# Kernel tuning notes

Hardware: AMD Instinct MI355X
Metric: run time of the kernel (lower is better)

## Reference

```python
import jax, jax.numpy as jnp
import numpy as np

B, T, D = 2, 4096, 2048
H, DI = 4, 64

def setup_inputs() -> dict:
    key = jax.random.key(0)
    k1, k2, k3, k4 = jax.random.split(key, 4)
    x = jax.random.normal(k1, (B, T, D), dtype=jnp.float32)
    # nn.Linear(in, out) weight applied as x @ W with W shaped [in, out]
    Wq = jax.random.normal(k2, (D, H * DI), dtype=jnp.float32) * (1.0 / np.sqrt(D))
    Wk = jax.random.normal(k3, (D, DI), dtype=jnp.float32) * (1.0 / np.sqrt(D))
    Ww = jax.random.normal(k4, (D, H), dtype=jnp.float32) * (1.0 / np.sqrt(D))
    return {"x": x, "Wq": Wq, "Wk": Wk, "Ww": Ww}

def reference(x, Wq, Wk, Ww):
    Bv, Tv, _ = x.shape
    queries = (x @ Wq).reshape(Bv, Tv, H, DI)   # [B,T,H,DI]
    keys = x @ Wk                                # [B,S,DI]
    weights = x @ Ww                             # [B,T,H]
    dots = jnp.einsum('bthd,bsd->bths', queries, keys)  # [B,T,H,S]
    activated = jax.nn.relu(dots)
    # per-head weight then head-reduction: sum_h w[b,t,h] * relu(dots)[b,t,h,s]
    index_scores = jnp.einsum('bths,bth->bts', activated, weights)
    return index_scores
```

## Files before the change

### kernel.cpp

```cpp
#include <hip/hip_runtime.h>
#include <hip/hip_bf16.h>

#define Bdim 2
#define Tdim 4096
#define Ddim 2048
#define Hdim 4
#define DIdim 64
#define NQ 256
#define NCAT 324
#define NPAD 384
#define Mdim 8192

typedef __attribute__((ext_vector_type(8))) short bf16x8;
typedef __attribute__((ext_vector_type(4))) float f32x4;

__device__ __forceinline__ unsigned short f2bf(float f) {
    unsigned int u = __builtin_bit_cast(unsigned int, f);
    u += 0x7fffu + ((u >> 16) & 1u);
    return (unsigned short)(u >> 16);
}
__device__ __forceinline__ float bf2f(unsigned short h) {
    unsigned int u = ((unsigned int)h) << 16;
    return __builtin_bit_cast(float, u);
}

__global__ __launch_bounds__(256) void pack_w(const float* __restrict__ Wq,
                                              const float* __restrict__ Wk,
                                              const float* __restrict__ Ww,
                                              unsigned short* __restrict__ WcatT) {
    const int n0 = blockIdx.x * 64;
    const int d0 = blockIdx.y * 64;
    __shared__ float tile[64][65];
    const int t = threadIdx.x;
#pragma unroll
    for (int i = 0; i < 16; ++i) {
        int flat = i * 256 + t;
        int r = flat >> 6;
        int c = flat & 63;
        int n = n0 + c, d = d0 + r;
        float v;
        if (n < NQ)            v = Wq[(size_t)d * NQ + n];
        else if (n < NQ + 64)  v = Wk[(size_t)d * DIdim + (n - NQ)];
        else if (n < NCAT)     v = Ww[(size_t)d * Hdim + (n - NQ - 64)];
        else                   v = 0.0f;
        tile[r][c] = v;
    }
    __syncthreads();
#pragma unroll
    for (int i = 0; i < 16; ++i) {
        int flat = i * 256 + t;
        int nn = flat >> 6;
        int dd = flat & 63;
        WcatT[(size_t)(n0 + nn) * Ddim + d0 + dd] = f2bf(tile[dd][nn]);
    }
}

#define BM 128
#define BN 64
#define BK 64

__global__ __launch_bounds__(256) void proj_gemm(const float* __restrict__ x,
                                                 const unsigned short* __restrict__ WcatT,
                                                 unsigned short* __restrict__ QKW) {
    __shared__ __align__(16) unsigned char lds[BM * BK * 2 + BN * BK * 2];
    const int m0 = blockIdx.y * BM;
    const int n0 = blockIdx.x * BN;
    const int tid = threadIdx.x;
    const int lane = tid & 63;
    const int wave = tid >> 6;

    f32x4 acc[2][4];
#pragma unroll
    for (int ts = 0; ts < 2; ++ts)
#pragma unroll
        for (int ns = 0; ns < 4; ++ns)
            acc[ts][ns] = (f32x4){0.f, 0.f, 0.f, 0.f};

    const int lrow = lane & 15;
    const int kgrp = lane >> 4;

    for (int k0 = 0; k0 < Ddim; k0 += BK) {
        __syncthreads();
#pragma unroll
        for (int i = 0; i < 8; ++i) {
            int flat = i * 256 + tid;
            int r = flat >> 4;
            int c4 = flat & 15;
            const float4 v = *reinterpret_cast<const float4*>(
                &x[(size_t)(m0 + r) * Ddim + k0 + c4 * 4]);
            unsigned int p0 = (unsigned int)f2bf(v.x) | ((unsigned int)f2bf(v.y) << 16);
            unsigned int p1 = (unsigned int)f2bf(v.z) | ((unsigned int)f2bf(v.w) << 16);
            int byte = r * 128 + c4 * 8;
            byte ^= (r & 7) << 4;
            *reinterpret_cast<uint2*>(&lds[byte]) = make_uint2(p0, p1);
        }
#pragma unroll
        for (int i = 0; i < 2; ++i) {
            int flat = i * 256 + tid;
            int n = flat >> 3;
            int k8 = flat & 7;
            const int4 v = *reinterpret_cast<const int4*>(
                &WcatT[(size_t)(n0 + n) * Ddim + k0 + k8 * 8]);
            int byte = n * 128 + k8 * 16;
            byte ^= (n & 7) << 4;
            *reinterpret_cast<int4*>(&lds[BM * BK * 2 + byte]) = v;
        }
        __syncthreads();
#pragma unroll
        for (int ks = 0; ks < 2; ++ks) {
            bf16x8 a[2], bb[4];
#pragma unroll
            for (int ts = 0; ts < 2; ++ts) {
                int r = wave * 32 + ts * 16 + lrow;
                int byte = r * 128 + (ks * 32 + 8 * kgrp) * 2;
                byte ^= (r & 7) << 4;
                a[ts] = *reinterpret_cast<const bf16x8*>(&lds[byte]);
            }
#pragma unroll
            for (int ns = 0; ns < 4; ++ns) {
                int n = ns * 16 + lrow;
                int byte = n * 128 + (ks * 32 + 8 * kgrp) * 2;
                byte ^= (n & 7) << 4;
                bb[ns] = *reinterpret_cast<const bf16x8*>(&lds[BM * BK * 2 + byte]);
            }
#pragma unroll
            for (int ts = 0; ts < 2; ++ts)
#pragma unroll
                for (int ns = 0; ns < 4; ++ns)
                    acc[ts][ns] = __builtin_amdgcn_mfma_f32_16x16x32_bf16(
                        a[ts], bb[ns], acc[ts][ns], 0, 0, 0);
        }
    }
#pragma unroll
    for (int ts = 0; ts < 2; ++ts)
#pragma unroll
        for (int ns = 0; ns < 4; ++ns)
#pragma unroll
            for (int j = 0; j < 4; ++j) {
                int r = m0 + wave * 32 + ts * 16 + kgrp * 4 + j;
                int c = n0 + ns * 16 + lrow;
                QKW[(size_t)r * NPAD + c] = f2bf(acc[ts][ns][j]);
            }
}

__global__ __launch_bounds__(256) void indexer(const unsigned short* __restrict__ QKW,
                                               float* __restrict__ out) {
    const int st = blockIdx.x;
    const int tt = blockIdx.y;
    const int b  = blockIdx.z;
    const int tid = threadIdx.x;
    const int lane = tid & 63;
    const int wave = tid >> 6;
    const int lrow = lane & 15;
    const int kgrp = lane >> 4;
    const int kcol = 8 * kgrp;

    bf16x8 kf[8][2];
#pragma unroll
    for (int ss = 0; ss < 8; ++ss)
#pragma unroll
        for (int ks = 0; ks < 2; ++ks) {
            size_t row = (size_t)(b * Tdim + st * 128 + ss * 16 + lrow);
            kf[ss][ks] = *reinterpret_cast<const bf16x8*>(
                &QKW[row * NPAD + NQ + ks * 32 + kcol]);
        }

    float wreg[2][4][4];
#pragma unroll
    for (int ts = 0; ts < 2; ++ts)
#pragma unroll
        for (int j = 0; j < 4; ++j) {
            int t = tt * 128 + wave * 32 + ts * 16 + kgrp * 4 + j;
            const unsigned short* wp = &QKW[(size_t)(b * Tdim + t) * NPAD + NQ + 64];
#pragma unroll
            for (int h = 0; h < Hdim; ++h) wreg[ts][j][h] = bf2f(wp[h]);
        }

    f32x4 oacc[2][8];
#pragma unroll
    for (int ts = 0; ts < 2; ++ts)
#pragma unroll
        for (int ss = 0; ss < 8; ++ss)
            oacc[ts][ss] = (f32x4){0.f, 0.f, 0.f, 0.f};

#pragma unroll
    for (int h = 0; h < Hdim; ++h) {
        bf16x8 qf[2][2];
#pragma unroll
        for (int ts = 0; ts < 2; ++ts)
#pragma unroll
            for (int ks = 0; ks < 2; ++ks) {
                size_t row = (size_t)(b * Tdim + tt * 128 + wave * 32 + ts * 16 + lrow);
                qf[ts][ks] = *reinterpret_cast<const bf16x8*>(
                    &QKW[row * NPAD + h * DIdim + ks * 32 + kcol]);
            }
#pragma unroll
        for (int ss = 0; ss < 8; ++ss) {
            f32x4 d[2];
            d[0] = (f32x4){0.f, 0.f, 0.f, 0.f};
            d[1] = (f32x4){0.f, 0.f, 0.f, 0.f};
#pragma unroll
            for (int ks = 0; ks < 2; ++ks)
#pragma unroll
                for (int ts = 0; ts < 2; ++ts)
                    d[ts] = __builtin_amdgcn_mfma_f32_16x16x32_bf16(
                        qf[ts][ks], kf[ss][ks], d[ts], 0, 0, 0);
#pragma unroll
            for (int ts = 0; ts < 2; ++ts)
#pragma unroll
                for (int j = 0; j < 4; ++j)
                    oacc[ts][ss][j] += wreg[ts][j][h] * fmaxf(d[ts][j], 0.f);
        }
    }

#pragma unroll
    for (int ts = 0; ts < 2; ++ts)
#pragma unroll
        for (int ss = 0; ss < 8; ++ss)
#pragma unroll
            for (int j = 0; j < 4; ++j) {
                int t = tt * 128 + wave * 32 + ts * 16 + kgrp * 4 + j;
                int s = st * 128 + ss * 16 + lrow;
                out[((size_t)b * Tdim + t) * Tdim + s] = oacc[ts][ss][j];
            }
}

extern "C" void kernel_launch(void* const* d_in, const int* in_sizes, int n_in,
                              void* d_out, int out_size, void* d_ws, size_t ws_size,
                              hipStream_t stream) {
    const float* x  = (const float*)d_in[0];
    const float* Wq = (const float*)d_in[1];
    const float* Wk = (const float*)d_in[2];
    const float* Ww = (const float*)d_in[3];
    float* out = (float*)d_out;

    unsigned short* WcatT = (unsigned short*)d_ws;
    unsigned short* QKW   = (unsigned short*)((char*)d_ws + (size_t)NPAD * Ddim * 2);

    pack_w<<<dim3(NPAD / 64, Ddim / 64), 256, 0, stream>>>(Wq, Wk, Ww, WcatT);
    proj_gemm<<<dim3(NPAD / BN, Mdim / BM), 256, 0, stream>>>(x, WcatT, QKW);
    indexer<<<dim3(Tdim / 128, Tdim / 128, Bdim), 256, 0, stream>>>(QKW, out);
}
```

Measured before the change: 260.6 us.

## Pre-convert x to bf16, async LDS-load projection GEMM, split indexer across 8 waves

Adds a separate kernel that converts x to bf16 once into workspace, and a new projection GEMM that stages tiles with global_load_lds direct-to-LDS copies using a 32x192 tile. The indexer now runs 512 threads, with each wave covering half the s-range; Q fragments for all heads are hoisted into registers, weights are read as one vector load, and output uses nontemporal stores. This is meant to cut conversion work inside the GEMM inner loop and improve indexer occupancy and write behaviour. In exchange it adds an extra pass over x and needs more workspace; the old GEMM is kept as a fallback when workspace is too small.

```diff
diff --git a/kernel.cpp b/kernel.cpp
--- a/kernel.cpp
+++ b/kernel.cpp
@@ -22,6 +22,28 @@
 __device__ __forceinline__ float bf2f(unsigned short h) {
     unsigned int u = ((unsigned int)h) << 16;
     return __builtin_bit_cast(float, u);
+}
+
+__device__ __forceinline__ void gload16(const void* g, void* l) {
+    __builtin_amdgcn_global_load_lds(
+        (const __attribute__((address_space(1))) unsigned int*)g,
+        (__attribute__((address_space(3))) unsigned int*)l, 16, 0, 0);
+}
+
+__global__ __launch_bounds__(256) void convert_x(const float* __restrict__ x,
+                                                 unsigned short* __restrict__ xb) {
+    const size_t N8 = (size_t)Mdim * Ddim / 8;
+    for (size_t u = (size_t)blockIdx.x * 256 + threadIdx.x; u < N8;
+         u += (size_t)gridDim.x * 256) {
+        const float4 v0 = *reinterpret_cast<const float4*>(&x[u * 8]);
+        const float4 v1 = *reinterpret_cast<const float4*>(&x[u * 8 + 4]);
+        uint4 o;
+        o.x = (unsigned int)f2bf(v0.x) | ((unsigned int)f2bf(v0.y) << 16);
+        o.y = (unsigned int)f2bf(v0.z) | ((unsigned int)f2bf(v0.w) << 16);
+        o.z = (unsigned int)f2bf(v1.x) | ((unsigned int)f2bf(v1.y) << 16);
+        o.w = (unsigned int)f2bf(v1.z) | ((unsigned int)f2bf(v1.w) << 16);
+        *reinterpret_cast<uint4*>(&xb[u * 8]) = o;
+    }
 }
 
 __global__ __launch_bounds__(256) void pack_w(const float* __restrict__ Wq,
@@ -55,30 +77,101 @@
     }
 }
 
-#define BM 128
-#define BN 64
+#define BM2 32
+#define BN2 192
 #define BK 64
 
+__global__ __launch_bounds__(256) void proj_gemm2(const unsigned short* __restrict__ xb,
+                                                  const unsigned short* __restrict__ WcatT,
+                                                  unsigned short* __restrict__ QKW) {
+    __shared__ __align__(16) unsigned char lds[(BM2 + BN2) * BK * 2];
+    const int n0 = blockIdx.x * BN2;
+    const int m0 = blockIdx.y * BM2;
+    const int tid = threadIdx.x;
+    const int lane = tid & 63;
+    const int wave = tid >> 6;
+    const int lrow = lane & 15;
+    const int kgrp = lane >> 4;
+
+    f32x4 acc[2][3];
+#pragma unroll
+    for (int ts = 0; ts < 2; ++ts)
+#pragma unroll
+        for (int ns = 0; ns < 3; ++ns)
+            acc[ts][ns] = (f32x4){0.f, 0.f, 0.f, 0.f};
+
+    for (int k0 = 0; k0 < Ddim; k0 += BK) {
+        __syncthreads();
+        {
+            int flat = tid;
+            int r = flat >> 3, c = flat & 7;
+            int cs = c ^ (r & 7);
+            gload16(&xb[(size_t)(m0 + r) * Ddim + k0 + cs * 8], &lds[flat * 16]);
+        }
+#pragma unroll
+        for (int i = 0; i < 6; ++i) {
+            int flat = i * 256 + tid;
+            int n = flat >> 3, c = flat & 7;
+            int cs = c ^ (n & 7);
+            gload16(&WcatT[(size_t)(n0 + n) * Ddim + k0 + cs * 8],
+                    &lds[BM2 * BK * 2 + flat * 16]);
+        }
+        __syncthreads();
+#pragma unroll
+        for (int ks = 0; ks < 2; ++ks) {
+            bf16x8 a[2], bb[3];
+#pragma unroll
+            for (int ts = 0; ts < 2; ++ts) {
+                int r = ts * 16 + lrow;
+                int c = (ks * 4 + kgrp) ^ (r & 7);
+                a[ts] = *reinterpret_cast<const bf16x8*>(&lds[r * 128 + c * 16]);
+            }
+#pragma unroll
+            for (int ns = 0; ns < 3; ++ns) {
+                int n = wave * 48 + ns * 16 + lrow;
+                int c = (ks * 4 + kgrp) ^ (n & 7);
+                bb[ns] = *reinterpret_cast<const bf16x8*>(
+                    &lds[BM2 * BK * 2 + n * 128 + c * 16]);
+            }
+#pragma unroll
+            for (int ts = 0; ts < 2; ++ts)
+#pragma unroll
+                for (int ns = 0; ns < 3; ++ns)
+                    acc[ts][ns] = __builtin_amdgcn_mfma_f32_16x16x32_bf16(
+                        a[ts], bb[ns], acc[ts][ns], 0, 0, 0);
+        }
+    }
+#pragma unroll
+    for (int ts = 0; ts < 2; ++ts)
+#pragma unroll
+        for (int ns = 0; ns < 3; ++ns)
+#pragma unroll
+            for (int j = 0; j < 4; ++j) {
+                int r = m0 + ts * 16 + kgrp * 4 + j;
+                int c = n0 + wave * 48 + ns * 16 + lrow;
+                QKW[(size_t)r * NPAD + c] = f2bf(acc[ts][ns][j]);
+            }
+}
+
+#define BMf 128
+#define BNf 64
 __global__ __launch_bounds__(256) void proj_gemm(const float* __restrict__ x,
                                                  const unsigned short* __restrict__ WcatT,
                                                  unsigned short* __restrict__ QKW) {
-    __shared__ __align__(16) unsigned char lds[BM * BK * 2 + BN * BK * 2];
-    const int m0 = blockIdx.y * BM;
-    const int n0 = blockIdx.x * BN;
+    __shared__ __align__(16) unsigned char lds[BMf * BK * 2 + BNf * BK * 2];
+    const int m0 = blockIdx.y * BMf;
+    const int n0 = blockIdx.x * BNf;
     const int tid = threadIdx.x;
     const int lane = tid & 63;
     const int wave = tid >> 6;
-
     f32x4 acc[2][4];
 #pragma unroll
     for (int ts = 0; ts < 2; ++ts)
 #pragma unroll
         for (int ns = 0; ns < 4; ++ns)
             acc[ts][ns] = (f32x4){0.f, 0.f, 0.f, 0.f};
-
     const int lrow = lane & 15;
     const int kgrp = lane >> 4;
-
     for (int k0 = 0; k0 < Ddim; k0 += BK) {
         __syncthreads();
 #pragma unroll
@@ -103,7 +196,7 @@
                 &WcatT[(size_t)(n0 + n) * Ddim + k0 + k8 * 8]);
             int byte = n * 128 + k8 * 16;
             byte ^= (n & 7) << 4;
-            *reinterpret_cast<int4*>(&lds[BM * BK * 2 + byte]) = v;
+            *reinterpret_cast<int4*>(&lds[BMf * BK * 2 + byte]) = v;
         }
         __syncthreads();
 #pragma unroll
@@ -121,7 +214,7 @@
                 int n = ns * 16 + lrow;
                 int byte = n * 128 + (ks * 32 + 8 * kgrp) * 2;
                 byte ^= (n & 7) << 4;
-                bb[ns] = *reinterpret_cast<const bf16x8*>(&lds[BM * BK * 2 + byte]);
+                bb[ns] = *reinterpret_cast<const bf16x8*>(&lds[BMf * BK * 2 + byte]);
             }
 #pragma unroll
             for (int ts = 0; ts < 2; ++ts)
@@ -143,59 +236,68 @@
             }
 }
 
-__global__ __launch_bounds__(256) void indexer(const unsigned short* __restrict__ QKW,
-                                               float* __restrict__ out) {
+__global__ __launch_bounds__(512) void indexer2(const unsigned short* __restrict__ QKW,
+                                                float* __restrict__ out) {
     const int st = blockIdx.x;
     const int tt = blockIdx.y;
     const int b  = blockIdx.z;
     const int tid = threadIdx.x;
     const int lane = tid & 63;
     const int wave = tid >> 6;
+    const int wt  = wave >> 1;
+    const int wsb = wave & 1;
     const int lrow = lane & 15;
     const int kgrp = lane >> 4;
     const int kcol = 8 * kgrp;
-
-    bf16x8 kf[8][2];
-#pragma unroll
-    for (int ss = 0; ss < 8; ++ss)
+    const size_t rowBase = (size_t)b * Tdim;
+
+    bf16x8 kf[4][2];
+#pragma unroll
+    for (int ss = 0; ss < 4; ++ss)
 #pragma unroll
         for (int ks = 0; ks < 2; ++ks) {
-            size_t row = (size_t)(b * Tdim + st * 128 + ss * 16 + lrow);
+            size_t row = rowBase + st * 128 + wsb * 64 + ss * 16 + lrow;
             kf[ss][ks] = *reinterpret_cast<const bf16x8*>(
                 &QKW[row * NPAD + NQ + ks * 32 + kcol]);
         }
 
+    bf16x8 qf[4][2][2];
+#pragma unroll
+    for (int h = 0; h < Hdim; ++h)
+#pragma unroll
+        for (int ts = 0; ts < 2; ++ts)
+#pragma unroll
+            for (int ks = 0; ks < 2; ++ks) {
+                size_t row = rowBase + tt * 128 + wt * 32 + ts * 16 + lrow;
+                qf[h][ts][ks] = *reinterpret_cast<const bf16x8*>(
+                    &QKW[row * NPAD + h * DIdim + ks * 32 + kcol]);
+            }
+
     float wreg[2][4][4];
 #pragma unroll
     for (int ts = 0; ts < 2; ++ts)
 #pragma unroll
         for (int j = 0; j < 4; ++j) {
-            int t = tt * 128 + wave * 32 + ts * 16 + kgrp * 4 + j;
-            const unsigned short* wp = &QKW[(size_t)(b * Tdim + t) * NPAD + NQ + 64];
-#pragma unroll
-            for (int h = 0; h < Hdim; ++h) wreg[ts][j][h] = bf2f(wp[h]);
-        }
-
-    f32x4 oacc[2][8];
-#pragma unroll
-    for (int ts = 0; ts < 2; ++ts)
-#pragma unroll
-        for (int ss = 0; ss < 8; ++ss)
+            int t = tt * 128 + wt * 32 + ts * 16 + kgrp * 4 + j;
+            const uint2 wp = *reinterpret_cast<const uint2*>(
+                &QKW[(rowBase + t) * NPAD + NQ + 64]);
+            wreg[ts][j][0] = bf2f((unsigned short)(wp.x & 0xffff));
+            wreg[ts][j][1] = bf2f((unsigned short)(wp.x >> 16));
+            wreg[ts][j][2] = bf2f((unsigned short)(wp.y & 0xffff));
+            wreg[ts][j][3] = bf2f((unsigned short)(wp.y >> 16));
+        }
+
+    f32x4 oacc[2][4];
+#pragma unroll
+    for (int ts = 0; ts < 2; ++ts)
+#pragma unroll
+        for (int ss = 0; ss < 4; ++ss)
             oacc[ts][ss] = (f32x4){0.f, 0.f, 0.f, 0.f};
 
 #pragma unroll
-    for (int h = 0; h < Hdim; ++h) {
-        bf16x8 qf[2][2];
-#pragma unroll
-        for (int ts = 0; ts < 2; ++ts)
-#pragma unroll
-            for (int ks = 0; ks < 2; ++ks) {
-                size_t row = (size_t)(b * Tdim + tt * 128 + wave * 32 + ts * 16 + lrow);
-                qf[ts][ks] = *reinterpret_cast<const bf16x8*>(
-                    &QKW[row * NPAD + h * DIdim + ks * 32 + kcol]);
-            }
-#pragma unroll
-        for (int ss = 0; ss < 8; ++ss) {
+    for (int ss = 0; ss < 4; ++ss)
+#pragma unroll
+        for (int h = 0; h < Hdim; ++h) {
             f32x4 d[2];
             d[0] = (f32x4){0.f, 0.f, 0.f, 0.f};
             d[1] = (f32x4){0.f, 0.f, 0.f, 0.f};
@@ -204,24 +306,25 @@
 #pragma unroll
                 for (int ts = 0; ts < 2; ++ts)
                     d[ts] = __builtin_amdgcn_mfma_f32_16x16x32_bf16(
-                        qf[ts][ks], kf[ss][ks], d[ts], 0, 0, 0);
+                        qf[h][ts][ks], kf[ss][ks], d[ts], 0, 0, 0);
 #pragma unroll
             for (int ts = 0; ts < 2; ++ts)
 #pragma unroll
                 for (int j = 0; j < 4; ++j)
-                    oacc[ts][ss][j] += wreg[ts][j][h] * fmaxf(d[ts][j], 0.f);
-        }
-    }
-
-#pragma unroll
-    for (int ts = 0; ts < 2; ++ts)
-#pragma unroll
-        for (int ss = 0; ss < 8; ++ss)
+                    oacc[ts][ss][j] = fmaf(wreg[ts][j][h], fmaxf(d[ts][j], 0.f),
+                                           oacc[ts][ss][j]);
+        }
+
+#pragma unroll
+    for (int ts = 0; ts < 2; ++ts)
+#pragma unroll
+        for (int ss = 0; ss < 4; ++ss)
 #pragma unroll
             for (int j = 0; j < 4; ++j) {
-                int t = tt * 128 + wave * 32 + ts * 16 + kgrp * 4 + j;
-                int s = st * 128 + ss * 16 + lrow;
-                out[((size_t)b * Tdim + t) * Tdim + s] = oacc[ts][ss][j];
+                int t = tt * 128 + wt * 32 + ts * 16 + kgrp * 4 + j;
+                int s = st * 128 + wsb * 64 + ss * 16 + lrow;
+                __builtin_nontemporal_store(oacc[ts][ss][j],
+                                            &out[(rowBase + t) * Tdim + s]);
             }
 }
 
@@ -236,8 +339,16 @@
 
     unsigned short* WcatT = (unsigned short*)d_ws;
     unsigned short* QKW   = (unsigned short*)((char*)d_ws + (size_t)NPAD * Ddim * 2);
+    const size_t qkw_bytes = (size_t)Mdim * NPAD * 2;
+    unsigned short* xb = (unsigned short*)((char*)QKW + qkw_bytes);
+    const size_t need = (size_t)NPAD * Ddim * 2 + qkw_bytes + (size_t)Mdim * Ddim * 2;
 
     pack_w<<<dim3(NPAD / 64, Ddim / 64), 256, 0, stream>>>(Wq, Wk, Ww, WcatT);
-    proj_gemm<<<dim3(NPAD / BN, Mdim / BM), 256, 0, stream>>>(x, WcatT, QKW);
-    indexer<<<dim3(Tdim / 128, Tdim / 128, Bdim), 256, 0, stream>>>(QKW, out);
-}
+    if (ws_size >= need) {
+        convert_x<<<2048, 256, 0, stream>>>(x, xb);
+        proj_gemm2<<<dim3(NPAD / BN2, Mdim / BM2), 256, 0, stream>>>(xb, WcatT, QKW);
+    } else {
+        proj_gemm<<<dim3(NPAD / BNf, Mdim / BMf), 256, 0, stream>>>(x, WcatT, QKW);
+    }
+    indexer2<<<dim3(Tdim / 128, Tdim / 128, Bdim), 512, 0, stream>>>(QKW, out);
+}
```

New measurement: 263.8 us. Within noise of the previous version (+1.2%).

## Pre-convert x to bf16, double-buffer projection GEMM with direct LDS loads, retile indexer

Applied to the files above, without the earlier changes.

Adds a separate kernel that converts x to bf16 once. The projection GEMM is rewritten with 32x192 tiles, 512 threads, and a double-buffered LDS pipeline fed by global_load_lds. The indexer now stages key tiles through LDS and splits each block across 8 waves. It also packs the head weights, raises MFMA priority and writes output with nontemporal stores. The cost is an extra launch and a full bf16 round trip of x through global memory.

```diff
diff --git a/kernel.cpp b/kernel.cpp
--- a/kernel.cpp
+++ b/kernel.cpp
@@ -22,6 +22,33 @@
 __device__ __forceinline__ float bf2f(unsigned short h) {
     unsigned int u = ((unsigned int)h) << 16;
     return __builtin_bit_cast(float, u);
+}
+__device__ __forceinline__ float wget(uint2 w, int h) {
+    unsigned int u = (h & 2) ? w.y : w.x;
+    unsigned int v = (h & 1) ? (u & 0xffff0000u) : (u << 16);
+    return __builtin_bit_cast(float, v);
+}
+
+__device__ __forceinline__ void gload16(const void* g, void* l) {
+    __builtin_amdgcn_global_load_lds(
+        (const __attribute__((address_space(1))) unsigned int*)g,
+        (__attribute__((address_space(3))) unsigned int*)l, 16, 0, 0);
+}
+
+__global__ __launch_bounds__(256) void convert_x(const float* __restrict__ x,
+                                                 unsigned short* __restrict__ xb) {
+    const size_t N8 = (size_t)Mdim * Ddim / 8;
+    for (size_t u = (size_t)blockIdx.x * 256 + threadIdx.x; u < N8;
+         u += (size_t)gridDim.x * 256) {
+        const float4 v0 = *reinterpret_cast<const float4*>(&x[u * 8]);
+        const float4 v1 = *reinterpret_cast<const float4*>(&x[u * 8 + 4]);
+        uint4 o;
+        o.x = (unsigned int)f2bf(v0.x) | ((unsigned int)f2bf(v0.y) << 16);
+        o.y = (unsigned int)f2bf(v0.z) | ((unsigned int)f2bf(v0.w) << 16);
+        o.z = (unsigned int)f2bf(v1.x) | ((unsigned int)f2bf(v1.y) << 16);
+        o.w = (unsigned int)f2bf(v1.z) | ((unsigned int)f2bf(v1.w) << 16);
+        *reinterpret_cast<uint4*>(&xb[u * 8]) = o;
+    }
 }
 
 __global__ __launch_bounds__(256) void pack_w(const float* __restrict__ Wq,
@@ -55,173 +82,173 @@
     }
 }
 
-#define BM 128
-#define BN 64
-#define BK 64
-
-__global__ __launch_bounds__(256) void proj_gemm(const float* __restrict__ x,
-                                                 const unsigned short* __restrict__ WcatT,
-                                                 unsigned short* __restrict__ QKW) {
-    __shared__ __align__(16) unsigned char lds[BM * BK * 2 + BN * BK * 2];
-    const int m0 = blockIdx.y * BM;
-    const int n0 = blockIdx.x * BN;
+#define PBM 32
+#define PBN 192
+#define PBK 64
+#define ABYTES (PBM * PBK * 2)
+#define BBYTES (PBN * PBK * 2)
+#define BUFBYTES (ABYTES + BBYTES)
+
+__global__ __launch_bounds__(512) void proj_gemm3(const unsigned short* __restrict__ xb,
+                                                  const unsigned short* __restrict__ WcatT,
+                                                  unsigned short* __restrict__ QKW) {
+    __shared__ __align__(16) unsigned char lds[2 * BUFBYTES];
+    const int n0 = blockIdx.x * PBN;
+    const int m0 = blockIdx.y * PBM;
     const int tid = threadIdx.x;
     const int lane = tid & 63;
-    const int wave = tid >> 6;
-
-    f32x4 acc[2][4];
-#pragma unroll
-    for (int ts = 0; ts < 2; ++ts)
-#pragma unroll
-        for (int ns = 0; ns < 4; ++ns)
-            acc[ts][ns] = (f32x4){0.f, 0.f, 0.f, 0.f};
-
+    const int wm = (tid >> 6) >> 2;
+    const int wn = (tid >> 6) & 3;
     const int lrow = lane & 15;
     const int kgrp = lane >> 4;
 
-    for (int k0 = 0; k0 < Ddim; k0 += BK) {
+    f32x4 acc[3];
+#pragma unroll
+    for (int ns = 0; ns < 3; ++ns) acc[ns] = (f32x4){0.f, 0.f, 0.f, 0.f};
+
+    auto stage = [&](unsigned char* buf, int k0) {
+        if (tid < 256) {
+            int r = tid >> 3, c = tid & 7;
+            int cs = c ^ (r & 7);
+            gload16(&xb[(size_t)(m0 + r) * Ddim + k0 + cs * 8], buf + tid * 16);
+        }
+#pragma unroll
+        for (int i = 0; i < 3; ++i) {
+            int flat = i * 512 + tid;
+            int n = flat >> 3, c = flat & 7;
+            int cs = c ^ (n & 7);
+            gload16(&WcatT[(size_t)(n0 + n) * Ddim + k0 + cs * 8],
+                    buf + ABYTES + flat * 16);
+        }
+    };
+
+    stage(lds, 0);
+    __syncthreads();
+    int cur = 0;
+    for (int k0 = 0; k0 < Ddim; k0 += PBK) {
+        unsigned char* bc = lds + cur * BUFBYTES;
+        unsigned char* bn = lds + (cur ^ 1) * BUFBYTES;
+        if (k0 + PBK < Ddim) stage(bn, k0 + PBK);
+#pragma unroll
+        for (int ks = 0; ks < 2; ++ks) {
+            int r = wm * 16 + lrow;
+            int ca = (ks * 4 + kgrp) ^ (r & 7);
+            bf16x8 a = *reinterpret_cast<const bf16x8*>(bc + r * 128 + ca * 16);
+            bf16x8 bb[3];
+#pragma unroll
+            for (int ns = 0; ns < 3; ++ns) {
+                int n = wn * 48 + ns * 16 + lrow;
+                int cb = (ks * 4 + kgrp) ^ (n & 7);
+                bb[ns] = *reinterpret_cast<const bf16x8*>(bc + ABYTES + n * 128 + cb * 16);
+            }
+#pragma unroll
+            for (int ns = 0; ns < 3; ++ns)
+                acc[ns] = __builtin_amdgcn_mfma_f32_16x16x32_bf16(a, bb[ns], acc[ns], 0, 0, 0);
+        }
         __syncthreads();
-#pragma unroll
-        for (int i = 0; i < 8; ++i) {
-            int flat = i * 256 + tid;
-            int r = flat >> 4;
-            int c4 = flat & 15;
-            const float4 v = *reinterpret_cast<const float4*>(
-                &x[(size_t)(m0 + r) * Ddim + k0 + c4 * 4]);
-            unsigned int p0 = (unsigned int)f2bf(v.x) | ((unsigned int)f2bf(v.y) << 16);
-            unsigned int p1 = (unsigned int)f2bf(v.z) | ((unsigned int)f2bf(v.w) << 16);
-            int byte = r * 128 + c4 * 8;
-            byte ^= (r & 7) << 4;
-            *reinterpret_cast<uint2*>(&lds[byte]) = make_uint2(p0, p1);
-        }
-#pragma unroll
-        for (int i = 0; i < 2; ++i) {
-            int flat = i * 256 + tid;
-            int n = flat >> 3;
-            int k8 = flat & 7;
-            const int4 v = *reinterpret_cast<const int4*>(
-                &WcatT[(size_t)(n0 + n) * Ddim + k0 + k8 * 8]);
-            int byte = n * 128 + k8 * 16;
-            byte ^= (n & 7) << 4;
-            *reinterpret_cast<int4*>(&lds[BM * BK * 2 + byte]) = v;
-        }
-        __syncthreads();
-#pragma unroll
-        for (int ks = 0; ks < 2; ++ks) {
-            bf16x8 a[2], bb[4];
-#pragma unroll
-            for (int ts = 0; ts < 2; ++ts) {
-                int r = wave * 32 + ts * 16 + lrow;
-                int byte = r * 128 + (ks * 32 + 8 * kgrp) * 2;
-                byte ^= (r & 7) << 4;
-                a[ts] = *reinterpret_cast<const bf16x8*>(&lds[byte]);
-            }
-#pragma unroll
-            for (int ns = 0; ns < 4; ++ns) {
-                int n = ns * 16 + lrow;
-                int byte = n * 128 + (ks * 32 + 8 * kgrp) * 2;
-                byte ^= (n & 7) << 4;
-                bb[ns] = *reinterpret_cast<const bf16x8*>(&lds[BM * BK * 2 + byte]);
-            }
-#pragma unroll
-            for (int ts = 0; ts < 2; ++ts)
-#pragma unroll
-                for (int ns = 0; ns < 4; ++ns)
-                    acc[ts][ns] = __builtin_amdgcn_mfma_f32_16x16x32_bf16(
-                        a[ts], bb[ns], acc[ts][ns], 0, 0, 0);
-        }
-    }
-#pragma unroll
-    for (int ts = 0; ts < 2; ++ts)
-#pragma unroll
-        for (int ns = 0; ns < 4; ++ns)
-#pragma unroll
-            for (int j = 0; j < 4; ++j) {
-                int r = m0 + wave * 32 + ts * 16 + kgrp * 4 + j;
-                int c = n0 + ns * 16 + lrow;
-                QKW[(size_t)r * NPAD + c] = f2bf(acc[ts][ns][j]);
-            }
-}
-
-__global__ __launch_bounds__(256) void indexer(const unsigned short* __restrict__ QKW,
-                                               float* __restrict__ out) {
+        cur ^= 1;
+    }
+#pragma unroll
+    for (int ns = 0; ns < 3; ++ns)
+#pragma unroll
+        for (int j = 0; j < 4; ++j) {
+            int r = m0 + wm * 16 + kgrp * 4 + j;
+            int c = n0 + wn * 48 + ns * 16 + lrow;
+            QKW[(size_t)r * NPAD + c] = f2bf(acc[ns][j]);
+        }
+}
+
+__global__ __launch_bounds__(512) void indexer3(const unsigned short* __restrict__ QKW,
+                                                float* __restrict__ out) {
+    __shared__ __align__(16) unsigned char klds[128 * 128];
     const int st = blockIdx.x;
     const int tt = blockIdx.y;
     const int b  = blockIdx.z;
     const int tid = threadIdx.x;
     const int lane = tid & 63;
     const int wave = tid >> 6;
+    const int wt  = wave >> 1;
+    const int wsb = wave & 1;
     const int lrow = lane & 15;
     const int kgrp = lane >> 4;
     const int kcol = 8 * kgrp;
-
-    bf16x8 kf[8][2];
-#pragma unroll
-    for (int ss = 0; ss < 8; ++ss)
-#pragma unroll
-        for (int ks = 0; ks < 2; ++ks) {
-            size_t row = (size_t)(b * Tdim + st * 128 + ss * 16 + lrow);
-            kf[ss][ks] = *reinterpret_cast<const bf16x8*>(
-                &QKW[row * NPAD + NQ + ks * 32 + kcol]);
-        }
-
-    float wreg[2][4][4];
+    const size_t rowBase = (size_t)b * Tdim;
+
+#pragma unroll
+    for (int i = 0; i < 2; ++i) {
+        int flat = i * 512 + tid;
+        int r = flat >> 3, c = flat & 7;
+        int cs = c ^ (r & 7);
+        gload16(&QKW[(rowBase + st * 128 + r) * NPAD + NQ + cs * 8], &klds[flat * 16]);
+    }
+
+    uint2 wpk[2][4];
 #pragma unroll
     for (int ts = 0; ts < 2; ++ts)
 #pragma unroll
         for (int j = 0; j < 4; ++j) {
-            int t = tt * 128 + wave * 32 + ts * 16 + kgrp * 4 + j;
-            const unsigned short* wp = &QKW[(size_t)(b * Tdim + t) * NPAD + NQ + 64];
-#pragma unroll
-            for (int h = 0; h < Hdim; ++h) wreg[ts][j][h] = bf2f(wp[h]);
-        }
-
-    f32x4 oacc[2][8];
+            int trow = tt * 128 + wt * 32 + ts * 16 + kgrp * 4 + j;
+            wpk[ts][j] = *reinterpret_cast<const uint2*>(
+                &QKW[(rowBase + trow) * NPAD + NQ + 64]);
+        }
+
+    f32x4 oacc[2][4];
 #pragma unroll
     for (int ts = 0; ts < 2; ++ts)
 #pragma unroll
-        for (int ss = 0; ss < 8; ++ss)
+        for (int ss = 0; ss < 4; ++ss)
             oacc[ts][ss] = (f32x4){0.f, 0.f, 0.f, 0.f};
 
+    __syncthreads();
+
+    const size_t qrow0 = rowBase + tt * 128 + wt * 32;
 #pragma unroll
     for (int h = 0; h < Hdim; ++h) {
         bf16x8 qf[2][2];
 #pragma unroll
         for (int ts = 0; ts < 2; ++ts)
 #pragma unroll
-            for (int ks = 0; ks < 2; ++ks) {
-                size_t row = (size_t)(b * Tdim + tt * 128 + wave * 32 + ts * 16 + lrow);
+            for (int ks = 0; ks < 2; ++ks)
                 qf[ts][ks] = *reinterpret_cast<const bf16x8*>(
-                    &QKW[row * NPAD + h * DIdim + ks * 32 + kcol]);
-            }
-#pragma unroll
-        for (int ss = 0; ss < 8; ++ss) {
+                    &QKW[(qrow0 + ts * 16 + lrow) * NPAD + h * DIdim + ks * 32 + kcol]);
+#pragma unroll
+        for (int ss = 0; ss < 4; ++ss) {
+            int rr = wsb * 64 + ss * 16 + lrow;
+            bf16x8 kf[2];
+#pragma unroll
+            for (int ks = 0; ks < 2; ++ks)
+                kf[ks] = *reinterpret_cast<const bf16x8*>(
+                    &klds[rr * 128 + ((ks * 4 + kgrp) ^ (rr & 7)) * 16]);
             f32x4 d[2];
             d[0] = (f32x4){0.f, 0.f, 0.f, 0.f};
             d[1] = (f32x4){0.f, 0.f, 0.f, 0.f};
+            __builtin_amdgcn_s_setprio(1);
 #pragma unroll
             for (int ks = 0; ks < 2; ++ks)
 #pragma unroll
                 for (int ts = 0; ts < 2; ++ts)
                     d[ts] = __builtin_amdgcn_mfma_f32_16x16x32_bf16(
-                        qf[ts][ks], kf[ss][ks], d[ts], 0, 0, 0);
+                        qf[ts][ks], kf[ks], d[ts], 0, 0, 0);
+            __builtin_amdgcn_s_setprio(0);
 #pragma unroll
             for (int ts = 0; ts < 2; ++ts)
 #pragma unroll
                 for (int j = 0; j < 4; ++j)
-                    oacc[ts][ss][j] += wreg[ts][j][h] * fmaxf(d[ts][j], 0.f);
+                    oacc[ts][ss][j] = fmaf(wget(wpk[ts][j], h),
+                                           fmaxf(d[ts][j], 0.f), oacc[ts][ss][j]);
         }
     }
 
 #pragma unroll
     for (int ts = 0; ts < 2; ++ts)
 #pragma unroll
-        for (int ss = 0; ss < 8; ++ss)
+        for (int ss = 0; ss < 4; ++ss)
 #pragma unroll
             for (int j = 0; j < 4; ++j) {
-                int t = tt * 128 + wave * 32 + ts * 16 + kgrp * 4 + j;
-                int s = st * 128 + ss * 16 + lrow;
-                out[((size_t)b * Tdim + t) * Tdim + s] = oacc[ts][ss][j];
+                int t = tt * 128 + wt * 32 + ts * 16 + kgrp * 4 + j;
+                int s = st * 128 + wsb * 64 + ss * 16 + lrow;
+                __builtin_nontemporal_store(oacc[ts][ss][j],
+                                            &out[(rowBase + t) * Tdim + s]);
             }
 }
 
@@ -236,8 +263,11 @@
 
     unsigned short* WcatT = (unsigned short*)d_ws;
     unsigned short* QKW   = (unsigned short*)((char*)d_ws + (size_t)NPAD * Ddim * 2);
-
+    const size_t qkw_bytes = (size_t)Mdim * NPAD * 2;
+    unsigned short* xb = (unsigned short*)((char*)QKW + qkw_bytes);
+
+    convert_x<<<2048, 256, 0, stream>>>(x, xb);
     pack_w<<<dim3(NPAD / 64, Ddim / 64), 256, 0, stream>>>(Wq, Wk, Ww, WcatT);
-    proj_gemm<<<dim3(NPAD / BN, Mdim / BM), 256, 0, stream>>>(x, WcatT, QKW);
-    indexer<<<dim3(Tdim / 128, Tdim / 128, Bdim), 256, 0, stream>>>(QKW, out);
-}
+    proj_gemm3<<<dim3(NPAD / PBN, Mdim / PBM), 512, 0, stream>>>(xb, WcatT, QKW);
+    indexer3<<<dim3(Tdim / 128, Tdim / 128, Bdim), 512, 0, stream>>>(QKW, out);
+}
```

Result: faster. 250.3 us (-3.9%).
